# Kernel tuning notes

Measured on AMD Instinct MI355X. Metric: run time of the kernel, lower is better.

The kernel has to match this reference:

```python
import jax, jax.numpy as jnp
import numpy as np
import math

D = 1024
H = 16
C = D // H
EPS = 1e-5

def layernorm(x, g, b):
    mu = jnp.mean(x, axis=-1, keepdims=True)
    var = jnp.mean(jnp.square(x - mu), axis=-1, keepdims=True)
    return (x - mu) * jax.lax.rsqrt(var + EPS) * g + b

def setup_inputs() -> dict:
    key = jax.random.key(0)
    ks = jax.random.split(key, 12)
    s = 1.0 / math.sqrt(D)
    inp = {
        "x": jax.random.normal(ks[0], (4, 2048, D), dtype=jnp.float32),
        "src_mask": jnp.ones((4, 2048), dtype=bool),
        "Wk": jax.random.normal(ks[1], (D, D), dtype=jnp.float32) * s,
        "Wq": jax.random.normal(ks[2], (D, D), dtype=jnp.float32) * s,
        "Wv": jax.random.normal(ks[3], (D, D), dtype=jnp.float32) * s,
        "Wfc": jax.random.normal(ks[4], (D, D), dtype=jnp.float32) * s,
        "bfc": jnp.zeros((D,), dtype=jnp.float32),
        "g1": jnp.ones((D,), dtype=jnp.float32),
        "b1": jnp.zeros((D,), dtype=jnp.float32),
        "g2": jnp.ones((D,), dtype=jnp.float32),
        "b2": jnp.zeros((D,), dtype=jnp.float32),
        "W1": jax.random.normal(ks[5], (D, 4 * D), dtype=jnp.float32) * s,
        "bf1": jnp.zeros((4 * D,), dtype=jnp.float32),
        "W2": jax.random.normal(ks[6], (4 * D, D), dtype=jnp.float32) * (1.0 / math.sqrt(4 * D)),
        "bf2": jnp.zeros((D,), dtype=jnp.float32),
    }
    return inp

def reference(x, src_mask, Wk, Wq, Wv, Wfc, bfc, g1, b1, g2, b2, W1, bf1, W2, bf2):
    b, s, _ = x.shape
    xl = layernorm(x, g1, b1)
    # self-attention (src_mask is unused in the original module)
    k = (xl @ Wk).reshape(b, s, H, C).transpose(0, 2, 1, 3)  # bhsc
    q = (xl @ Wq).reshape(b, s, H, C).transpose(0, 2, 1, 3)
    v = (xl @ Wv).reshape(b, s, H, C).transpose(0, 2, 1, 3)
    # NOTE: original multiplies by sqrt(c) (not divide) -- faithful quirk
    scores = jnp.einsum('bhqc,bhkc->bhqk', q, k) * math.sqrt(C)
    attn = jax.nn.softmax(scores, axis=-1)
    o = jnp.einsum('bhqk,bhkc->bhqc', attn, v)
    o = o.transpose(0, 2, 1, 3).reshape(b, s, D)
    ka = o @ Wfc + bfc
    x = ka + x
    xl2 = layernorm(x, g2, b2)
    ff = jax.nn.relu(xl2 @ W1 + bf1) @ W2 + bf2
    return ff + x
```

## Files before the change

kernel.cpp:

```cpp
#include <hip/hip_runtime.h>
#include <hip/hip_bf16.h>
#include <math.h>


typedef __hip_bfloat16 bf16_t;
typedef __bf16 bf16x8 __attribute__((ext_vector_type(8)));
typedef float f32x4 __attribute__((ext_vector_type(4)));

#define LN_EPS 1e-5f
#define QSCALE 11.541560327111707f

__device__ __forceinline__ void async_copy16(const bf16_t* g, bf16_t* l) {
  __builtin_amdgcn_global_load_lds(
      (const __attribute__((address_space(1))) void*)g,
      (__attribute__((address_space(3))) void*)l,
      16 , 0 , 0 );
}

__device__ __forceinline__ void split_bf16(float v, bf16_t& hi, bf16_t& lo) {
  hi = __float2bfloat16(v);
  lo = __float2bfloat16(v - __bfloat162float(hi));
}

template<bool SPLIT>
__global__ __launch_bounds__(256) void ln_kernel(
    const float* __restrict__ x, const float* __restrict__ g,
    const float* __restrict__ b, bf16_t* __restrict__ out_hi,
    bf16_t* __restrict__ out_lo)
{
  const int row = blockIdx.x;
  const int tid = threadIdx.x;
  const float4 v = *(const float4*)(x + (size_t)row * 1024 + tid * 4);
  float s  = v.x + v.y + v.z + v.w;
  float ss = v.x * v.x + v.y * v.y + v.z * v.z + v.w * v.w;
  for (int off = 32; off > 0; off >>= 1) {
    s  += __shfl_down(s, off);
    ss += __shfl_down(ss, off);
  }
  __shared__ float sb[4], ssb[4];
  const int wave = tid >> 6, lane = tid & 63;
  if (lane == 0) { sb[wave] = s; ssb[wave] = ss; }
  __syncthreads();
  const float tot  = sb[0] + sb[1] + sb[2] + sb[3];
  const float tots = ssb[0] + ssb[1] + ssb[2] + ssb[3];
  const float mu   = tot * (1.0f / 1024.0f);
  const float var  = tots * (1.0f / 1024.0f) - mu * mu;
  const float rstd = rsqrtf(var + LN_EPS);
  const float4 gv = *(const float4*)(g + tid * 4);
  const float4 bv = *(const float4*)(b + tid * 4);
  float y[4] = {(v.x - mu) * rstd * gv.x + bv.x,
                (v.y - mu) * rstd * gv.y + bv.y,
                (v.z - mu) * rstd * gv.z + bv.z,
                (v.w - mu) * rstd * gv.w + bv.w};
  bf16_t hi[4] __attribute__((aligned(8)));
  bf16_t lo[4] __attribute__((aligned(8)));
  #pragma unroll
  for (int i = 0; i < 4; i++) split_bf16(y[i], hi[i], lo[i]);
  uint2 ph, pl;
  __builtin_memcpy(&ph, hi, 8);
  *(uint2*)(out_hi + (size_t)row * 1024 + tid * 4) = ph;
  if (SPLIT) {
    __builtin_memcpy(&pl, lo, 8);
    *(uint2*)(out_lo + (size_t)row * 1024 + tid * 4) = pl;
  }
}

template<bool SPLIT>
__global__ __launch_bounds__(256) void wtrans_kernel(
    const float* __restrict__ W, bf16_t* __restrict__ WT_hi,
    bf16_t* __restrict__ WT_lo, int K, int N)
{
  __shared__ float t[32][33];
  const int n0 = blockIdx.x * 32, k0 = blockIdx.y * 32;
  const int tx = threadIdx.x & 31, ty = threadIdx.x >> 5;
  #pragma unroll
  for (int r = ty; r < 32; r += 8)
    t[r][tx] = W[(size_t)(k0 + r) * N + n0 + tx];
  __syncthreads();
  #pragma unroll
  for (int r = ty; r < 32; r += 8) {
    const float v = t[tx][r];
    bf16_t hi, lo;
    split_bf16(v, hi, lo);
    WT_hi[(size_t)(n0 + r) * K + k0 + tx] = hi;
    if (SPLIT) WT_lo[(size_t)(n0 + r) * K + k0 + tx] = lo;
  }
}

template<bool BIAS, bool RELU, bool RESID, bool OUTBF>
__global__ __launch_bounds__(256) void gemm_kernel(
    const bf16_t* __restrict__ A, const bf16_t* __restrict__ BT,
    const float* __restrict__ bias, const float* __restrict__ resid,
    float* __restrict__ outF, bf16_t* __restrict__ outB,
    int M, int N, int K)
{
  __shared__ __align__(16) bf16_t As[128 * 32];
  __shared__ __align__(16) bf16_t Bs[128 * 32];
  const int nblk = N >> 7;
  const int bm = blockIdx.x / nblk;
  const int bn = blockIdx.x % nblk;
  const int tid  = threadIdx.x;
  const int wave = tid >> 6;
  const int lane = tid & 63;
  const int l15  = lane & 15;
  const int quad = lane >> 4;
  const int wm = wave >> 1, wn = wave & 1;

  const bf16_t* aG = A  + (size_t)(bm * 128 + wave * 32 + (lane >> 2)) * K + (lane & 3) * 8;
  const bf16_t* bG = BT + (size_t)(bn * 128 + wave * 32 + (lane >> 2)) * K + (lane & 3) * 8;
  bf16_t* aL0 = &As[(wave * 32) * 32];
  bf16_t* aL1 = &As[(wave * 32 + 16) * 32];
  bf16_t* bL0 = &Bs[(wave * 32) * 32];
  bf16_t* bL1 = &Bs[(wave * 32 + 16) * 32];

  f32x4 acc[4][4];
  #pragma unroll
  for (int i = 0; i < 4; i++)
    #pragma unroll
    for (int j = 0; j < 4; j++) acc[i][j] = (f32x4){0.f, 0.f, 0.f, 0.f};

  for (int kt = 0; kt < K; kt += 32) {
    async_copy16(aG + kt, aL0);
    async_copy16(aG + kt + (size_t)16 * K, aL1);
    async_copy16(bG + kt, bL0);
    async_copy16(bG + kt + (size_t)16 * K, bL1);
    __syncthreads();
    bf16x8 af[4], bfr[4];
    #pragma unroll
    for (int i = 0; i < 4; i++)
      af[i]  = *(const bf16x8*)&As[(wm * 64 + i * 16 + l15) * 32 + quad * 8];
    #pragma unroll
    for (int j = 0; j < 4; j++)
      bfr[j] = *(const bf16x8*)&Bs[(wn * 64 + j * 16 + l15) * 32 + quad * 8];
    #pragma unroll
    for (int i = 0; i < 4; i++)
      #pragma unroll
      for (int j = 0; j < 4; j++)
        acc[i][j] = __builtin_amdgcn_mfma_f32_16x16x32_bf16(af[i], bfr[j], acc[i][j], 0, 0, 0);
    __syncthreads();
  }

  const int gm0 = bm * 128 + wm * 64 + quad * 4;
  const int gn0 = bn * 128 + wn * 64 + l15;
  #pragma unroll
  for (int i = 0; i < 4; i++) {
    #pragma unroll
    for (int j = 0; j < 4; j++) {
      const int gn = gn0 + j * 16;
      const float bz = BIAS ? bias[gn] : 0.0f;
      #pragma unroll
      for (int r = 0; r < 4; r++) {
        const int gm = gm0 + i * 16 + r;
        float v = acc[i][j][r] + bz;
        if (RESID) v += resid[(size_t)gm * N + gn];
        if (RELU)  v = fmaxf(v, 0.0f);
        if (OUTBF) outB[(size_t)gm * N + gn] = __float2bfloat16(v);
        else       outF[(size_t)gm * N + gn] = v;
      }
    }
  }
}

__global__ __launch_bounds__(256) void gemm_split_kernel(
    const bf16_t* __restrict__ Ah, const bf16_t* __restrict__ Al,
    const bf16_t* __restrict__ Bh, const bf16_t* __restrict__ Bl,
    bf16_t* __restrict__ out_hi, bf16_t* __restrict__ out_lo,
    int M, int N, int K)
{
  __shared__ __align__(16) bf16_t AsH[128 * 32];
  __shared__ __align__(16) bf16_t AsL[128 * 32];
  __shared__ __align__(16) bf16_t BsH[128 * 32];
  __shared__ __align__(16) bf16_t BsL[128 * 32];
  const int nblk = N >> 7;
  const int bm = blockIdx.x / nblk;
  const int bn = blockIdx.x % nblk;
  const int tid  = threadIdx.x;
  const int wave = tid >> 6;
  const int lane = tid & 63;
  const int l15  = lane & 15;
  const int quad = lane >> 4;
  const int wm = wave >> 1, wn = wave & 1;

  const size_t aOff = (size_t)(bm * 128 + wave * 32 + (lane >> 2)) * K + (lane & 3) * 8;
  const size_t bOff = (size_t)(bn * 128 + wave * 32 + (lane >> 2)) * K + (lane & 3) * 8;
  const int ldsOff0 = (wave * 32) * 32;
  const int ldsOff1 = (wave * 32 + 16) * 32;

  f32x4 acc[4][4];
  #pragma unroll
  for (int i = 0; i < 4; i++)
    #pragma unroll
    for (int j = 0; j < 4; j++) acc[i][j] = (f32x4){0.f, 0.f, 0.f, 0.f};

  for (int kt = 0; kt < K; kt += 32) {
    async_copy16(Ah + aOff + kt, &AsH[ldsOff0]);
    async_copy16(Ah + aOff + kt + (size_t)16 * K, &AsH[ldsOff1]);
    async_copy16(Al + aOff + kt, &AsL[ldsOff0]);
    async_copy16(Al + aOff + kt + (size_t)16 * K, &AsL[ldsOff1]);
    async_copy16(Bh + bOff + kt, &BsH[ldsOff0]);
    async_copy16(Bh + bOff + kt + (size_t)16 * K, &BsH[ldsOff1]);
    async_copy16(Bl + bOff + kt, &BsL[ldsOff0]);
    async_copy16(Bl + bOff + kt + (size_t)16 * K, &BsL[ldsOff1]);
    __syncthreads();
    bf16x8 afH[4], afL[4], bfH[4], bfL[4];
    #pragma unroll
    for (int i = 0; i < 4; i++) {
      const int o = (wm * 64 + i * 16 + l15) * 32 + quad * 8;
      afH[i] = *(const bf16x8*)&AsH[o];
      afL[i] = *(const bf16x8*)&AsL[o];
    }
    #pragma unroll
    for (int j = 0; j < 4; j++) {
      const int o = (wn * 64 + j * 16 + l15) * 32 + quad * 8;
      bfH[j] = *(const bf16x8*)&BsH[o];
      bfL[j] = *(const bf16x8*)&BsL[o];
    }
    #pragma unroll
    for (int i = 0; i < 4; i++)
      #pragma unroll
      for (int j = 0; j < 4; j++) {
        acc[i][j] = __builtin_amdgcn_mfma_f32_16x16x32_bf16(afH[i], bfH[j], acc[i][j], 0, 0, 0);
        acc[i][j] = __builtin_amdgcn_mfma_f32_16x16x32_bf16(afH[i], bfL[j], acc[i][j], 0, 0, 0);
        acc[i][j] = __builtin_amdgcn_mfma_f32_16x16x32_bf16(afL[i], bfH[j], acc[i][j], 0, 0, 0);
      }
    __syncthreads();
  }

  const int gm0 = bm * 128 + wm * 64 + quad * 4;
  const int gn0 = bn * 128 + wn * 64 + l15;
  #pragma unroll
  for (int i = 0; i < 4; i++)
    #pragma unroll
    for (int j = 0; j < 4; j++) {
      const int gn = gn0 + j * 16;
      const float scale = (gn < 1024) ? QSCALE : 1.0f;
      #pragma unroll
      for (int r = 0; r < 4; r++) {
        const int gm = gm0 + i * 16 + r;
        bf16_t hi, lo;
        split_bf16(acc[i][j][r] * scale, hi, lo);
        out_hi[(size_t)gm * N + gn] = hi;
        out_lo[(size_t)gm * N + gn] = lo;
      }
    }
}

__global__ __launch_bounds__(256) void attn_kernel(
    const bf16_t* __restrict__ qkH,
    const bf16_t* __restrict__ qkL,
    const bf16_t* __restrict__ vT,
    bf16_t* __restrict__ o)
{
  const int qt = blockIdx.x;
  const int h  = blockIdx.y;
  const int b  = blockIdx.z;
  const int wave = threadIdx.x >> 6;
  const int lane = threadIdx.x & 63;
  const int l15  = lane & 15;
  const int quad = lane >> 4;
  const int sw   = l15 & 7;
  const int qrowA = qt * 128 + wave * 32;
  const int qrowB = qrowA + 16;

  __shared__ __align__(16) bf16_t KhL[64 * 64];
  __shared__ __align__(16) bf16_t KlL[64 * 64];
  __shared__ __align__(16) bf16_t VtL[64 * 64];
  __shared__ __align__(16) bf16_t Pl[4][32 * 64];

  const size_t tok0 = (size_t)b * 2048;
  const size_t qoffA = (tok0 + qrowA + l15) * 2048 + h * 64;
  const size_t qoffB = (tok0 + qrowB + l15) * 2048 + h * 64;
  const bf16x8 aA0H = *(const bf16x8*)(qkH + qoffA + quad * 8);
  const bf16x8 aA1H = *(const bf16x8*)(qkH + qoffA + 32 + quad * 8);
  const bf16x8 aA0L = *(const bf16x8*)(qkL + qoffA + quad * 8);
  const bf16x8 aA1L = *(const bf16x8*)(qkL + qoffA + 32 + quad * 8);
  const bf16x8 aB0H = *(const bf16x8*)(qkH + qoffB + quad * 8);
  const bf16x8 aB1H = *(const bf16x8*)(qkH + qoffB + 32 + quad * 8);
  const bf16x8 aB0L = *(const bf16x8*)(qkL + qoffB + quad * 8);
  const bf16x8 aB1L = *(const bf16x8*)(qkL + qoffB + 32 + quad * 8);

  const int kOff = 1024 + h * 64;
  const int rsub = lane >> 3;
  const int csw  = (lane & 7) ^ (rsub & 7);

  f32x4 mxA = (f32x4){-3.0e38f, -3.0e38f, -3.0e38f, -3.0e38f};
  f32x4 mxB = mxA;
  for (int kb = 0; kb < 2048; kb += 64) {
    #pragma unroll
    for (int j = 0; j < 2; j++) {
      const int row0 = wave * 16 + j * 8;
      async_copy16(qkH + (tok0 + kb + row0 + rsub) * 2048 + kOff + csw * 8,
                   &KhL[row0 * 64]);
    }
    __syncthreads();
    #pragma unroll
    for (int t = 0; t < 4; t++) {
      const int base = (t * 16 + l15) * 64;
      const bf16x8 bh0 = *(const bf16x8*)&KhL[base + ((quad) ^ sw) * 8];
      const bf16x8 bh1 = *(const bf16x8*)&KhL[base + ((4 + quad) ^ sw) * 8];
      f32x4 accA = (f32x4){0.f, 0.f, 0.f, 0.f};
      f32x4 accB = accA;
      accA = __builtin_amdgcn_mfma_f32_16x16x32_bf16(aA0H, bh0, accA, 0, 0, 0);
      accA = __builtin_amdgcn_mfma_f32_16x16x32_bf16(aA1H, bh1, accA, 0, 0, 0);
      accB = __builtin_amdgcn_mfma_f32_16x16x32_bf16(aB0H, bh0, accB, 0, 0, 0);
      accB = __builtin_amdgcn_mfma_f32_16x16x32_bf16(aB1H, bh1, accB, 0, 0, 0);
      #pragma unroll
      for (int r = 0; r < 4; r++) {
        mxA[r] = fmaxf(mxA[r], accA[r]);
        mxB[r] = fmaxf(mxB[r], accB[r]);
      }
    }
    __syncthreads();
  }
  f32x4 negMA, negMB;
  #pragma unroll
  for (int r = 0; r < 4; r++) {
    float mA = mxA[r], mB = mxB[r];
    mA = fmaxf(mA, __shfl_xor(mA, 1)); mB = fmaxf(mB, __shfl_xor(mB, 1));
    mA = fmaxf(mA, __shfl_xor(mA, 2)); mB = fmaxf(mB, __shfl_xor(mB, 2));
    mA = fmaxf(mA, __shfl_xor(mA, 4)); mB = fmaxf(mB, __shfl_xor(mB, 4));
    mA = fmaxf(mA, __shfl_xor(mA, 8)); mB = fmaxf(mB, __shfl_xor(mB, 8));
    negMA[r] = -(mA + 4.0f);
    negMB[r] = -(mB + 4.0f);
  }

  f32x4 OfA[4], OfB[4];
  f32x4 lsumA = (f32x4){0.f, 0.f, 0.f, 0.f};
  f32x4 lsumB = lsumA;
  #pragma unroll
  for (int c = 0; c < 4; c++) { OfA[c] = lsumA; OfB[c] = lsumA; }
  bf16_t* pw = &Pl[wave][0];

  for (int kb = 0; kb < 2048; kb += 64) {
    #pragma unroll
    for (int j = 0; j < 2; j++) {
      const int row0 = wave * 16 + j * 8;
      const size_t krow = tok0 + kb + row0 + rsub;
      async_copy16(qkH + krow * 2048 + kOff + csw * 8, &KhL[row0 * 64]);
      async_copy16(qkL + krow * 2048 + kOff + csw * 8, &KlL[row0 * 64]);
      async_copy16(vT + (size_t)(h * 64 + row0 + rsub) * 8192 + tok0 + kb + csw * 8,
                   &VtL[row0 * 64]);
    }
    __syncthreads();

    #pragma unroll
    for (int t = 0; t < 4; t++) {
      const int base = (t * 16 + l15) * 64;
      const bf16x8 bh0 = *(const bf16x8*)&KhL[base + ((quad) ^ sw) * 8];
      const bf16x8 bh1 = *(const bf16x8*)&KhL[base + ((4 + quad) ^ sw) * 8];
      const bf16x8 bl0 = *(const bf16x8*)&KlL[base + ((quad) ^ sw) * 8];
      const bf16x8 bl1 = *(const bf16x8*)&KlL[base + ((4 + quad) ^ sw) * 8];
      f32x4 accA = negMA;
      f32x4 accB = negMB;
      accA = __builtin_amdgcn_mfma_f32_16x16x32_bf16(aA0H, bh0, accA, 0, 0, 0);
      accA = __builtin_amdgcn_mfma_f32_16x16x32_bf16(aA1H, bh1, accA, 0, 0, 0);
      accA = __builtin_amdgcn_mfma_f32_16x16x32_bf16(aA0H, bl0, accA, 0, 0, 0);
      accA = __builtin_amdgcn_mfma_f32_16x16x32_bf16(aA1H, bl1, accA, 0, 0, 0);
      accA = __builtin_amdgcn_mfma_f32_16x16x32_bf16(aA0L, bh0, accA, 0, 0, 0);
      accA = __builtin_amdgcn_mfma_f32_16x16x32_bf16(aA1L, bh1, accA, 0, 0, 0);
      accB = __builtin_amdgcn_mfma_f32_16x16x32_bf16(aB0H, bh0, accB, 0, 0, 0);
      accB = __builtin_amdgcn_mfma_f32_16x16x32_bf16(aB1H, bh1, accB, 0, 0, 0);
      accB = __builtin_amdgcn_mfma_f32_16x16x32_bf16(aB0H, bl0, accB, 0, 0, 0);
      accB = __builtin_amdgcn_mfma_f32_16x16x32_bf16(aB1H, bl1, accB, 0, 0, 0);
      accB = __builtin_amdgcn_mfma_f32_16x16x32_bf16(aB0L, bh0, accB, 0, 0, 0);
      accB = __builtin_amdgcn_mfma_f32_16x16x32_bf16(aB1L, bh1, accB, 0, 0, 0);
      #pragma unroll
      for (int r = 0; r < 4; r++) {
        const float pA = __builtin_amdgcn_exp2f(accA[r]);
        const float pB = __builtin_amdgcn_exp2f(accB[r]);
        lsumA[r] += pA;
        lsumB[r] += pB;
        const int RA = quad * 4 + r;
        const int RB = 16 + RA;
        pw[RA * 64 + (((t * 2 + (l15 >> 3)) ^ (RA & 7)) * 8) + (l15 & 7)] =
            __float2bfloat16(pA);
        pw[RB * 64 + (((t * 2 + (l15 >> 3)) ^ (RB & 7)) * 8) + (l15 & 7)] =
            __float2bfloat16(pB);
      }
    }

    const bf16x8 paA0 = *(const bf16x8*)&pw[l15 * 64 + ((quad) ^ sw) * 8];
    const bf16x8 paA1 = *(const bf16x8*)&pw[l15 * 64 + ((4 + quad) ^ sw) * 8];
    const bf16x8 paB0 = *(const bf16x8*)&pw[(16 + l15) * 64 + ((quad) ^ sw) * 8];
    const bf16x8 paB1 = *(const bf16x8*)&pw[(16 + l15) * 64 + ((4 + quad) ^ sw) * 8];
    #pragma unroll
    for (int c = 0; c < 4; c++) {
      const int vb = (c * 16 + l15) * 64;
      const bf16x8 bv0 = *(const bf16x8*)&VtL[vb + ((quad) ^ sw) * 8];
      const bf16x8 bv1 = *(const bf16x8*)&VtL[vb + ((4 + quad) ^ sw) * 8];
      OfA[c] = __builtin_amdgcn_mfma_f32_16x16x32_bf16(paA0, bv0, OfA[c], 0, 0, 0);
      OfA[c] = __builtin_amdgcn_mfma_f32_16x16x32_bf16(paA1, bv1, OfA[c], 0, 0, 0);
      OfB[c] = __builtin_amdgcn_mfma_f32_16x16x32_bf16(paB0, bv0, OfB[c], 0, 0, 0);
      OfB[c] = __builtin_amdgcn_mfma_f32_16x16x32_bf16(paB1, bv1, OfB[c], 0, 0, 0);
    }
    __syncthreads();
  }

  float lrowA[4], lrowB[4];
  #pragma unroll
  for (int r = 0; r < 4; r++) {
    float cA = lsumA[r], cB = lsumB[r];
    cA += __shfl_xor(cA, 1); cB += __shfl_xor(cB, 1);
    cA += __shfl_xor(cA, 2); cB += __shfl_xor(cB, 2);
    cA += __shfl_xor(cA, 4); cB += __shfl_xor(cB, 4);
    cA += __shfl_xor(cA, 8); cB += __shfl_xor(cB, 8);
    lrowA[r] = cA; lrowB[r] = cB;
  }

  bf16_t* opA = o + (tok0 + qrowA) * 1024 + h * 64;
  bf16_t* opB = o + (tok0 + qrowB) * 1024 + h * 64;
  #pragma unroll
  for (int c = 0; c < 4; c++)
    #pragma unroll
    for (int r = 0; r < 4; r++) {
      opA[(size_t)(quad * 4 + r) * 1024 + c * 16 + l15] =
          __float2bfloat16(OfA[c][r] / lrowA[r]);
      opB[(size_t)(quad * 4 + r) * 1024 + c * 16 + l15] =
          __float2bfloat16(OfB[c][r] / lrowB[r]);
    }
}

extern "C" void kernel_launch(void* const* d_in, const int* in_sizes, int n_in,
                              void* d_out, int out_size, void* d_ws, size_t ws_size,
                              hipStream_t stream)
{
  (void)in_sizes; (void)n_in; (void)out_size; (void)ws_size;
  const float* x   = (const float*)d_in[0];
  const float* Wk  = (const float*)d_in[2];
  const float* Wq  = (const float*)d_in[3];
  const float* Wv  = (const float*)d_in[4];
  const float* Wfc = (const float*)d_in[5];
  const float* bfc = (const float*)d_in[6];
  const float* g1  = (const float*)d_in[7];
  const float* b1  = (const float*)d_in[8];
  const float* g2  = (const float*)d_in[9];
  const float* b2  = (const float*)d_in[10];
  const float* W1  = (const float*)d_in[11];
  const float* bf1 = (const float*)d_in[12];
  const float* W2  = (const float*)d_in[13];
  const float* bf2 = (const float*)d_in[14];
  float* out = (float*)d_out;

  char* ws = (char*)d_ws;
  bf16_t* xl_hi  = (bf16_t*)(ws + (0ull   << 20));
  bf16_t* oAtt   = xl_hi;
  bf16_t* xl_lo  = (bf16_t*)(ws + (16ull  << 20));
  bf16_t* vT     = xl_lo;
  bf16_t* xl2    = xl_lo;
  bf16_t* qk_hi  = (bf16_t*)(ws + (32ull  << 20));
  bf16_t* qk_lo  = (bf16_t*)(ws + (64ull  << 20));
  bf16_t* h1     = qk_hi;
  float*  x2     = (float*) (ws + (112ull << 20));
  bf16_t* Wqk_hi = (bf16_t*)(ws + (144ull << 20));
  bf16_t* Wqk_lo = (bf16_t*)(ws + (148ull << 20));
  bf16_t* WvT    = (bf16_t*)(ws + (152ull << 20));
  bf16_t* WfcT   = (bf16_t*)(ws + (154ull << 20));
  bf16_t* W1T    = (bf16_t*)(ws + (156ull << 20));
  bf16_t* W2T    = (bf16_t*)(ws + (164ull << 20));

  const dim3 blk(256);

  wtrans_kernel<true ><<<dim3(32, 32),  blk, 0, stream>>>(Wq,  Wqk_hi,               Wqk_lo,               1024, 1024);
  wtrans_kernel<true ><<<dim3(32, 32),  blk, 0, stream>>>(Wk,  Wqk_hi + 1024 * 1024, Wqk_lo + 1024 * 1024, 1024, 1024);
  wtrans_kernel<false><<<dim3(32, 32),  blk, 0, stream>>>(Wv,  WvT,  nullptr, 1024, 1024);
  wtrans_kernel<false><<<dim3(32, 32),  blk, 0, stream>>>(Wfc, WfcT, nullptr, 1024, 1024);
  wtrans_kernel<false><<<dim3(128, 32), blk, 0, stream>>>(W1,  W1T,  nullptr, 1024, 4096);
  wtrans_kernel<false><<<dim3(32, 128), blk, 0, stream>>>(W2,  W2T,  nullptr, 4096, 1024);

  ln_kernel<true><<<8192, blk, 0, stream>>>(x, g1, b1, xl_hi, xl_lo);

  gemm_split_kernel<<<64 * 16, blk, 0, stream>>>(
      xl_hi, xl_lo, Wqk_hi, Wqk_lo, qk_hi, qk_lo, 8192, 2048, 1024);

  gemm_kernel<false, false, false, true><<<8 * 64, blk, 0, stream>>>(
      WvT, xl_hi, nullptr, nullptr, nullptr, vT, 1024, 8192, 1024);

  attn_kernel<<<dim3(16, 16, 4), blk, 0, stream>>>(qk_hi, qk_lo, vT, oAtt);

  gemm_kernel<true, false, true, false><<<64 * 8, blk, 0, stream>>>(
      oAtt, WfcT, bfc, x, x2, nullptr, 8192, 1024, 1024);

  ln_kernel<false><<<8192, blk, 0, stream>>>(x2, g2, b2, xl2, nullptr);

  gemm_kernel<true, true, false, true><<<64 * 32, blk, 0, stream>>>(
      xl2, W1T, bf1, nullptr, nullptr, h1, 8192, 4096, 1024);

  gemm_kernel<true, false, true, false><<<64 * 8, blk, 0, stream>>>(
      h1, W2T, bf2, x2, out, nullptr, 8192, 1024, 4096);
}
```

Measured before the change: 736.2 us.

## Merge weight transposes into one launch and widen attention max-pass K tile

Replaces the six weight transpose/split launches with a single kernel that picks its source and destination matrix from the block index, cutting launch overhead. In the attention kernel, shared memory becomes one aliased buffer so the first (row-max) pass can load 256 keys per sync instead of 64. This gives four times fewer barriers and loads in that pass. Shared memory use stays about the same because the K, V and P buffers alias the larger key tile.

```diff
diff --git a/kernel.cpp b/kernel.cpp
--- a/kernel.cpp
+++ b/kernel.cpp
@@ -65,13 +65,35 @@
   }
 }
 
-template<bool SPLIT>
-__global__ __launch_bounds__(256) void wtrans_kernel(
-    const float* __restrict__ W, bf16_t* __restrict__ WT_hi,
-    bf16_t* __restrict__ WT_lo, int K, int N)
+__global__ __launch_bounds__(256) void wtrans_all_kernel(
+    const float* __restrict__ Wq, const float* __restrict__ Wk,
+    const float* __restrict__ Wv, const float* __restrict__ Wfc,
+    const float* __restrict__ W1, const float* __restrict__ W2,
+    bf16_t* __restrict__ WqkH, bf16_t* __restrict__ WqkL,
+    bf16_t* __restrict__ WvT, bf16_t* __restrict__ WfcT,
+    bf16_t* __restrict__ W1T, bf16_t* __restrict__ W2T)
 {
+  const int id = blockIdx.x;
+  const float* W; bf16_t* DH; bf16_t* DL = nullptr;
+  int K, N, n0, k0;
+  if (id < 4096) {
+    K = 1024; N = 1024;
+    const int local = id & 1023;
+    n0 = (local & 31) * 32; k0 = (local >> 5) * 32;
+    if (id < 1024)      { W = Wq;  DH = WqkH;                 DL = WqkL; }
+    else if (id < 2048) { W = Wk;  DH = WqkH + 1024 * 1024;   DL = WqkL + 1024 * 1024; }
+    else if (id < 3072) { W = Wv;  DH = WvT; }
+    else                { W = Wfc; DH = WfcT; }
+  } else if (id < 8192) {
+    const int local = id - 4096;
+    K = 1024; N = 4096; W = W1; DH = W1T;
+    n0 = (local & 127) * 32; k0 = (local >> 7) * 32;
+  } else {
+    const int local = id - 8192;
+    K = 4096; N = 1024; W = W2; DH = W2T;
+    n0 = (local & 31) * 32; k0 = (local >> 5) * 32;
+  }
   __shared__ float t[32][33];
-  const int n0 = blockIdx.x * 32, k0 = blockIdx.y * 32;
   const int tx = threadIdx.x & 31, ty = threadIdx.x >> 5;
   #pragma unroll
   for (int r = ty; r < 32; r += 8)
@@ -82,8 +104,8 @@
     const float v = t[tx][r];
     bf16_t hi, lo;
     split_bf16(v, hi, lo);
-    WT_hi[(size_t)(n0 + r) * K + k0 + tx] = hi;
-    if (SPLIT) WT_lo[(size_t)(n0 + r) * K + k0 + tx] = lo;
+    DH[(size_t)(n0 + r) * K + k0 + tx] = hi;
+    if (DL) DL[(size_t)(n0 + r) * K + k0 + tx] = lo;
   }
 }
 
@@ -262,10 +284,12 @@
   const int qrowA = qt * 128 + wave * 32;
   const int qrowB = qrowA + 16;
 
-  __shared__ __align__(16) bf16_t KhL[64 * 64];
-  __shared__ __align__(16) bf16_t KlL[64 * 64];
-  __shared__ __align__(16) bf16_t VtL[64 * 64];
-  __shared__ __align__(16) bf16_t Pl[4][32 * 64];
+  __shared__ __align__(16) bf16_t SMEM[20480];
+  bf16_t* Kbig = SMEM;
+  bf16_t* KhL  = SMEM;
+  bf16_t* KlL  = SMEM + 4096;
+  bf16_t* VtL  = SMEM + 8192;
+  bf16_t* pw   = SMEM + 12288 + wave * 2048;
 
   const size_t tok0 = (size_t)b * 2048;
   const size_t qoffA = (tok0 + qrowA + l15) * 2048 + h * 64;
@@ -285,19 +309,19 @@
 
   f32x4 mxA = (f32x4){-3.0e38f, -3.0e38f, -3.0e38f, -3.0e38f};
   f32x4 mxB = mxA;
-  for (int kb = 0; kb < 2048; kb += 64) {
-    #pragma unroll
-    for (int j = 0; j < 2; j++) {
-      const int row0 = wave * 16 + j * 8;
+  for (int kb = 0; kb < 2048; kb += 256) {
+    #pragma unroll
+    for (int j = 0; j < 8; j++) {
+      const int row0 = wave * 64 + j * 8;
       async_copy16(qkH + (tok0 + kb + row0 + rsub) * 2048 + kOff + csw * 8,
-                   &KhL[row0 * 64]);
-    }
-    __syncthreads();
-    #pragma unroll
-    for (int t = 0; t < 4; t++) {
+                   &Kbig[row0 * 64]);
+    }
+    __syncthreads();
+    #pragma unroll
+    for (int t = 0; t < 16; t++) {
       const int base = (t * 16 + l15) * 64;
-      const bf16x8 bh0 = *(const bf16x8*)&KhL[base + ((quad) ^ sw) * 8];
-      const bf16x8 bh1 = *(const bf16x8*)&KhL[base + ((4 + quad) ^ sw) * 8];
+      const bf16x8 bh0 = *(const bf16x8*)&Kbig[base + ((quad) ^ sw) * 8];
+      const bf16x8 bh1 = *(const bf16x8*)&Kbig[base + ((4 + quad) ^ sw) * 8];
       f32x4 accA = (f32x4){0.f, 0.f, 0.f, 0.f};
       f32x4 accB = accA;
       accA = __builtin_amdgcn_mfma_f32_16x16x32_bf16(aA0H, bh0, accA, 0, 0, 0);
@@ -329,7 +353,6 @@
   f32x4 lsumB = lsumA;
   #pragma unroll
   for (int c = 0; c < 4; c++) { OfA[c] = lsumA; OfB[c] = lsumA; }
-  bf16_t* pw = &Pl[wave][0];
 
   for (int kb = 0; kb < 2048; kb += 64) {
     #pragma unroll
@@ -460,12 +483,8 @@
 
   const dim3 blk(256);
 
-  wtrans_kernel<true ><<<dim3(32, 32),  blk, 0, stream>>>(Wq,  Wqk_hi,               Wqk_lo,               1024, 1024);
-  wtrans_kernel<true ><<<dim3(32, 32),  blk, 0, stream>>>(Wk,  Wqk_hi + 1024 * 1024, Wqk_lo + 1024 * 1024, 1024, 1024);
-  wtrans_kernel<false><<<dim3(32, 32),  blk, 0, stream>>>(Wv,  WvT,  nullptr, 1024, 1024);
-  wtrans_kernel<false><<<dim3(32, 32),  blk, 0, stream>>>(Wfc, WfcT, nullptr, 1024, 1024);
-  wtrans_kernel<false><<<dim3(128, 32), blk, 0, stream>>>(W1,  W1T,  nullptr, 1024, 4096);
-  wtrans_kernel<false><<<dim3(32, 128), blk, 0, stream>>>(W2,  W2T,  nullptr, 4096, 1024);
+  wtrans_all_kernel<<<12288, blk, 0, stream>>>(
+      Wq, Wk, Wv, Wfc, W1, W2, Wqk_hi, Wqk_lo, WvT, WfcT, W1T, W2T);
 
   ln_kernel<true><<<8192, blk, 0, stream>>>(x, g1, b1, xl_hi, xl_lo);
 
```

Result: no change. 722.4 us (-1.9%).
